# Performance work log

Measured on AMD Instinct MI355X. Metric: run time of the kernel, lower is better.

## Reference

```python
import jax, jax.numpy as jnp
import numpy as np

N_HEADS = 16
D_EMBED = 1024
HEAD_DIM = D_EMBED // N_HEADS


def setup_inputs() -> dict:
    key = jax.random.key(0)
    ks = jax.random.split(key, 9)
    s = 1.0 / np.sqrt(D_EMBED)
    def lin(kw, kb):
        W = jax.random.uniform(kw, (D_EMBED, D_EMBED), jnp.float32, -s, s)
        b = jax.random.uniform(kb, (D_EMBED,), jnp.float32, -s, s)
        return W, b
    q_w, q_b = lin(ks[0], ks[1])
    k_w, k_b = lin(ks[2], ks[3])
    v_w, v_b = lin(ks[4], ks[5])
    o_w, o_b = lin(ks[6], ks[7])
    x = jax.random.normal(ks[8], (4, 2048, D_EMBED), jnp.float32)
    return {"x": x, "q_w": q_w, "q_b": q_b, "k_w": k_w, "k_b": k_b,
            "v_w": v_w, "v_b": v_b, "o_w": o_w, "o_b": o_b}


def reference(x, q_w, q_b, k_w, k_b, v_w, v_b, o_w, o_b):
    B, S, _ = x.shape
    # projections; W stored as [in, out] so y = x @ W + b (matches nn.Linear math)
    def split_heads(y):
        return y.reshape(B, S, N_HEADS, HEAD_DIM).transpose(0, 2, 1, 3)  # [B,H,S,D]
    q = split_heads(x @ q_w + q_b)
    k = split_heads(x @ k_w + k_b)
    v = split_heads(x @ v_w + v_b)
    scale = 1.0 / np.sqrt(HEAD_DIM).astype(np.float32)
    scores = jnp.einsum('bhqd,bhkd->bhqk', q, k) * scale  # [B,H,S,S]
    weights = jax.nn.softmax(scores, axis=-1)
    attn = jnp.einsum('bhqk,bhkd->bhqd', weights, v)  # [B,H,S,D]
    attn = attn.transpose(0, 2, 1, 3).reshape(B, S, D_EMBED)
    return attn @ o_w + o_b
```

## Files before the change

kernel.cpp:

```cpp
#include <hip/hip_runtime.h>
#include <hip/hip_bf16.h>
#include <math.h>

typedef __attribute__((ext_vector_type(8))) short bf16x8;
typedef __attribute__((ext_vector_type(4))) float f32x4;

#define D_EMBED 1024
#define SEQ 2048
#define NH 16
#define HD 64
#define QSCALE 0.1803368801111204f

__device__ __forceinline__ short f2bf(float f) {
    union { float f; unsigned u; } v; v.f = f;
    return (short)((v.u + 0x7FFFu + ((v.u >> 16) & 1u)) >> 16);
}

__device__ __forceinline__ unsigned pk_bf16(float a, float b) {
#if __has_builtin(__builtin_amdgcn_cvt_pk_bf16_f32)
    typedef __attribute__((ext_vector_type(2))) __bf16 vbf2;
    union { vbf2 v; unsigned u; } c;
    c.v = __builtin_amdgcn_cvt_pk_bf16_f32(a, b);
    return c.u;
#else
    return (unsigned)(unsigned short)f2bf(a) | ((unsigned)(unsigned short)f2bf(b) << 16);
#endif
}

__device__ __forceinline__ float exp2f_(float x) {
#if __has_builtin(__builtin_amdgcn_exp2f)
    return __builtin_amdgcn_exp2f(x);
#else
    return __expf(x * 0.6931471805599453f);
#endif
}

typedef __attribute__((address_space(1))) const void gvoid_t;
typedef __attribute__((address_space(3))) void lvoid_t;
__device__ __forceinline__ void glds16(const void* g, void* l) {
    __builtin_amdgcn_global_load_lds((gvoid_t*)g, (lvoid_t*)l, 16, 0, 0);
}

__global__ __launch_bounds__(256) void xconv_kernel(const float* __restrict__ x,
                                                    short* __restrict__ xb)
{
    size_t i = ((size_t)blockIdx.x * 256 + threadIdx.x) * 8;
    float4 f0 = *(const float4*)(x + i);
    float4 f1 = *(const float4*)(x + i + 4);
    uint4 o;
    o.x = pk_bf16(f0.x, f0.y); o.y = pk_bf16(f0.z, f0.w);
    o.z = pk_bf16(f1.x, f1.y); o.w = pk_bf16(f1.z, f1.w);
    *(uint4*)(xb + i) = o;
}

__global__ __launch_bounds__(256) void wtrans_kernel(
    const float* __restrict__ w0, const float* __restrict__ w1,
    const float* __restrict__ w2, const float* __restrict__ w3,
    short* __restrict__ wt)
{
    __shared__ float tile[64][65];
    const float* W = (blockIdx.z == 0) ? w0 : (blockIdx.z == 1) ? w1
                   : (blockIdx.z == 2) ? w2 : w3;
    short* out = wt + (size_t)blockIdx.z * D_EMBED * D_EMBED;
    int k0 = blockIdx.x * 64, n0 = blockIdx.y * 64;
    #pragma unroll
    for (int i = 0; i < 16; i++) {
        int idx = threadIdx.x + i * 256; int r = idx >> 6, c = idx & 63;
        tile[r][c] = W[(size_t)(k0 + r) * D_EMBED + n0 + c];
    }
    __syncthreads();
    #pragma unroll
    for (int i = 0; i < 16; i++) {
        int idx = threadIdx.x + i * 256; int r = idx >> 6, c = idx & 63;
        out[(size_t)(n0 + r) * D_EMBED + k0 + c] = f2bf(tile[c][r]);
    }
}

__global__ __launch_bounds__(256) void gemm_qkv_kernel(
    const short* __restrict__ xb, const short* __restrict__ wt,
    const float* __restrict__ qb, const float* __restrict__ kb, const float* __restrict__ vb,
    short* __restrict__ qo, short* __restrict__ ko, short* __restrict__ vto)
{
    __shared__ __attribute__((aligned(16))) short As[128][32];
    __shared__ __attribute__((aligned(16))) short Bs[128][32];
    __shared__ __attribute__((aligned(16))) short Es[64][136];
    const int tid = threadIdx.x;
    const int lane = tid & 63, wv = tid >> 6;
    const int l16 = lane & 15, quad = lane >> 4;
    const int wm = (wv & 1) * 64, wn = (wv >> 1) * 64;
    const int m0 = blockIdx.y * 128, n0 = blockIdx.x * 128;

    const short* aptr0 = xb + (size_t)(m0 + (tid >> 2)) * D_EMBED + (tid & 3) * 8;
    const short* aptr1 = aptr0 + (size_t)64 * D_EMBED;
    const short* bptr0 = wt + (size_t)(n0 + (tid >> 2)) * D_EMBED + (tid & 3) * 8;
    const short* bptr1 = bptr0 + (size_t)64 * D_EMBED;
    char* aldsb = (char*)&As[0][0] + wv * 1024;
    char* bldsb = (char*)&Bs[0][0] + wv * 1024;

    f32x4 acc[4][4];
    #pragma unroll
    for (int a = 0; a < 4; a++)
        #pragma unroll
        for (int b = 0; b < 4; b++) acc[a][b] = (f32x4){0.f, 0.f, 0.f, 0.f};

    for (int k0 = 0; k0 < D_EMBED; k0 += 32) {
        __syncthreads();
        glds16(aptr0 + k0, aldsb);
        glds16(aptr1 + k0, aldsb + 4096);
        glds16(bptr0 + k0, bldsb);
        glds16(bptr1 + k0, bldsb + 4096);
        __syncthreads();
        bf16x8 af[4], bfr[4];
        #pragma unroll
        for (int mi = 0; mi < 4; mi++) af[mi]  = *(const bf16x8*)&As[wm + mi * 16 + l16][quad * 8];
        #pragma unroll
        for (int ni = 0; ni < 4; ni++) bfr[ni] = *(const bf16x8*)&Bs[wn + ni * 16 + l16][quad * 8];
        #pragma unroll
        for (int mi = 0; mi < 4; mi++)
            #pragma unroll
            for (int ni = 0; ni < 4; ni++)
                acc[mi][ni] = __builtin_amdgcn_mfma_f32_16x16x32_bf16(af[mi], bfr[ni], acc[mi][ni], 0, 0, 0);
    }

    const int zz = n0 >> 10;
    if (zz == 2) {
        const int b = m0 >> 11, st0 = m0 & 2047;
        const int hbase = (n0 & 1023) >> 6;
        #pragma unroll
        for (int h2 = 0; h2 < 2; h2++) {
            __syncthreads();
            if ((wv >> 1) == h2) {
                #pragma unroll
                for (int mi = 0; mi < 4; mi++) {
                    int sbase = (wv & 1) * 64 + mi * 16 + quad * 4;
                    #pragma unroll
                    for (int ni = 0; ni < 4; ni++) {
                        int d = ni * 16 + l16;
                        float bv = vb[(n0 & 1023) + h2 * 64 + d];
                        uint2 pw;
                        pw.x = pk_bf16(acc[mi][ni][0] + bv, acc[mi][ni][1] + bv);
                        pw.y = pk_bf16(acc[mi][ni][2] + bv, acc[mi][ni][3] + bv);
                        *(uint2*)&Es[d][sbase] = pw;
                    }
                }
            }
            __syncthreads();
            const int h = hbase + h2;
            #pragma unroll
            for (int j = 0; j < 4; j++) {
                int d = j * 16 + (tid >> 4);
                int sc = (tid & 15) * 8;
                bf16x8 vv = *(const bf16x8*)&Es[d][sc];
                *(bf16x8*)(vto + ((size_t)(b * NH + h) * HD + d) * SEQ + st0 + sc) = vv;
            }
        }
    } else {
        const int ncol0 = (n0 & 1023) + wn;
        const float* bias = (zz == 0) ? qb : kb;
        #pragma unroll
        for (int mi = 0; mi < 4; mi++)
            #pragma unroll
            for (int ni = 0; ni < 4; ni++)
                #pragma unroll
                for (int rg = 0; rg < 4; rg++) {
                    int row = m0 + wm + mi * 16 + quad * 4 + rg;
                    int col = ncol0 + ni * 16 + l16;
                    float v = acc[mi][ni][rg] + bias[col];
                    int b = row >> 11, s = row & 2047, h = col >> 6, d = col & 63;
                    if (zz == 0) qo[(((size_t)(b * NH + h)) * SEQ + s) * HD + d] = f2bf(v * QSCALE);
                    else         ko[(((size_t)(b * NH + h)) * SEQ + s) * HD + d] = f2bf(v);
                }
    }
}

__global__ __launch_bounds__(256) void flash_kernel(
    const short* __restrict__ Q, const short* __restrict__ K,
    const short* __restrict__ Vt, short* __restrict__ attn,
    short* __restrict__ Op0, short* __restrict__ Op1,
    float* __restrict__ lp0, float* __restrict__ lp1,
    int ktn, int mode)
{
    __shared__ __attribute__((aligned(16))) short Ks[64][64];
    __shared__ __attribute__((aligned(16))) short Vs[64][64];
    __shared__ __attribute__((aligned(16))) short Ps[4][64][72];
    const int bh = blockIdx.y, qt = blockIdx.x;
    const int kt0 = blockIdx.z * ktn;
    const int tid = threadIdx.x, lane = tid & 63, wv = tid >> 6;
    const int l16 = lane & 15, quad = lane >> 4;
    const int sw = l16 & 7;

    bf16x8 qf[4][2];
    #pragma unroll
    for (int g = 0; g < 4; g++) {
        const short* qp = Q + ((size_t)bh * SEQ + qt * 256 + wv * 64 + g * 16 + l16) * HD;
        qf[g][0] = *(const bf16x8*)(qp + quad * 8);
        qf[g][1] = *(const bf16x8*)(qp + 32 + quad * 8);
    }

    const int sr = tid >> 3;
    const int scg = (tid & 7) ^ (sr & 7);
    const short* kp0 = K  + ((size_t)bh * SEQ + sr) * HD + scg * 8;
    const short* vp0 = Vt + ((size_t)bh * HD + sr) * SEQ + scg * 8;
    char* kldsb = (char*)&Ks[0][0] + wv * 1024;
    char* vldsb = (char*)&Vs[0][0] + wv * 1024;

    float lsum[4] = {0.f, 0.f, 0.f, 0.f};
    f32x4 oacc[4][4];
    #pragma unroll
    for (int g = 0; g < 4; g++)
        #pragma unroll
        for (int di = 0; di < 4; di++) oacc[g][di] = (f32x4){0.f, 0.f, 0.f, 0.f};

    for (int kt = kt0; kt < kt0 + ktn; kt += 64) {
        __syncthreads();
        glds16(kp0 + (size_t)kt * HD, kldsb);
        glds16(kp0 + (size_t)(kt + 32) * HD, kldsb + 4096);
        glds16(vp0 + kt, vldsb);
        glds16(vp0 + (size_t)32 * SEQ + kt, vldsb + 4096);
        __syncthreads();

        bf16x8 kf[4][2];
        #pragma unroll
        for (int ni = 0; ni < 4; ni++) {
            kf[ni][0] = *(const bf16x8*)&Ks[ni * 16 + l16][((quad    ) ^ sw) * 8];
            kf[ni][1] = *(const bf16x8*)&Ks[ni * 16 + l16][((quad + 4) ^ sw) * 8];
        }

        #pragma unroll
        for (int g = 0; g < 4; g++) {
            f32x4 sacc[4];
            #pragma unroll
            for (int ni = 0; ni < 4; ni++) {
                sacc[ni] = (f32x4){0.f, 0.f, 0.f, 0.f};
                sacc[ni] = __builtin_amdgcn_mfma_f32_16x16x32_bf16(kf[ni][0], qf[g][0], sacc[ni], 0, 0, 0);
                sacc[ni] = __builtin_amdgcn_mfma_f32_16x16x32_bf16(kf[ni][1], qf[g][1], sacc[ni], 0, 0, 0);
            }
            short* prow = &Ps[wv][g * 16 + l16][0];
            float ps = 0.f;
            #pragma unroll
            for (int ni = 0; ni < 4; ni++) {
                float p0 = exp2f_(sacc[ni][0]);
                float p1 = exp2f_(sacc[ni][1]);
                float p2 = exp2f_(sacc[ni][2]);
                float p3 = exp2f_(sacc[ni][3]);
                ps += (p0 + p1) + (p2 + p3);
                uint2 pw; pw.x = pk_bf16(p0, p1); pw.y = pk_bf16(p2, p3);
                *(uint2*)(prow + ni * 16 + quad * 4) = pw;
            }
            lsum[g] += ps;
        }

        bf16x8 vf[4][2];
        #pragma unroll
        for (int di = 0; di < 4; di++) {
            vf[di][0] = *(const bf16x8*)&Vs[di * 16 + l16][((quad    ) ^ sw) * 8];
            vf[di][1] = *(const bf16x8*)&Vs[di * 16 + l16][((quad + 4) ^ sw) * 8];
        }
        #pragma unroll
        for (int g = 0; g < 4; g++) {
            const short* prow = &Ps[wv][g * 16 + l16][0];
            bf16x8 pf0 = *(const bf16x8*)(prow + quad * 8);
            bf16x8 pf1 = *(const bf16x8*)(prow + 32 + quad * 8);
            #pragma unroll
            for (int di = 0; di < 4; di++) {
                oacc[g][di] = __builtin_amdgcn_mfma_f32_16x16x32_bf16(pf0, vf[di][0], oacc[g][di], 0, 0, 0);
                oacc[g][di] = __builtin_amdgcn_mfma_f32_16x16x32_bf16(pf1, vf[di][1], oacc[g][di], 0, 0, 0);
            }
        }
    }

    const int b = bh >> 4, h = bh & 15;
    short* Oz = blockIdx.z ? Op1 : Op0;
    float* lz = blockIdx.z ? lp1 : lp0;
    #pragma unroll
    for (int g = 0; g < 4; g++) {
        float l = lsum[g];
        l += __shfl_xor(l, 16);
        l += __shfl_xor(l, 32);
        if (mode) {
            if (quad == 0) lz[(size_t)bh * SEQ + qt * 256 + wv * 64 + g * 16 + l16] = l;
            #pragma unroll
            for (int di = 0; di < 4; di++)
                #pragma unroll
                for (int rg = 0; rg < 4; rg++) {
                    int s = qt * 256 + wv * 64 + g * 16 + quad * 4 + rg;
                    int col = h * HD + di * 16 + l16;
                    Oz[((size_t)b * SEQ + s) * D_EMBED + col] = f2bf(oacc[g][di][rg]);
                }
        } else {
            float rl[4];
            #pragma unroll
            for (int rg = 0; rg < 4; rg++) rl[rg] = 1.0f / __shfl(l, quad * 4 + rg);
            #pragma unroll
            for (int di = 0; di < 4; di++)
                #pragma unroll
                for (int rg = 0; rg < 4; rg++) {
                    int s = qt * 256 + wv * 64 + g * 16 + quad * 4 + rg;
                    int col = h * HD + di * 16 + l16;
                    attn[((size_t)b * SEQ + s) * D_EMBED + col] = f2bf(oacc[g][di][rg] * rl[rg]);
                }
        }
    }
}

__global__ __launch_bounds__(256) void combine_kernel(
    const short* __restrict__ Op0, const short* __restrict__ Op1,
    const float* __restrict__ lp0, const float* __restrict__ lp1,
    short* __restrict__ attn)
{
    size_t i = (size_t)blockIdx.x * 256 + threadIdx.x;
    int r = (int)(i >> 7);
    int c8 = ((int)i & 127) * 8;
    int h = c8 >> 6, b = r >> 11, s = r & 2047;
    float l = lp0[(size_t)(b * NH + h) * SEQ + s] + lp1[(size_t)(b * NH + h) * SEQ + s];
    float rl = 1.0f / l;
    uint4 a0 = *(const uint4*)(Op0 + i * 8);
    uint4 a1 = *(const uint4*)(Op1 + i * 8);
    uint4 o;
    unsigned ua[4] = {a0.x, a0.y, a0.z, a0.w};
    unsigned ub[4] = {a1.x, a1.y, a1.z, a1.w};
    unsigned uo[4];
    #pragma unroll
    for (int j = 0; j < 4; j++) {
        union { unsigned u; float f; } f0l, f0h, f1l, f1h;
        f0l.u = (ua[j] & 0xffffu) << 16; f0h.u = ua[j] & 0xffff0000u;
        f1l.u = (ub[j] & 0xffffu) << 16; f1h.u = ub[j] & 0xffff0000u;
        uo[j] = pk_bf16((f0l.f + f1l.f) * rl, (f0h.f + f1h.f) * rl);
    }
    o.x = uo[0]; o.y = uo[1]; o.z = uo[2]; o.w = uo[3];
    *(uint4*)(attn + i * 8) = o;
}

__global__ __launch_bounds__(256) void gemm_out_kernel(
    const short* __restrict__ attn, const short* __restrict__ wt_o,
    const float* __restrict__ ob, float* __restrict__ out)
{
    __shared__ __attribute__((aligned(16))) short As[128][32];
    __shared__ __attribute__((aligned(16))) short Bs[128][32];
    const int tid = threadIdx.x;
    const int lane = tid & 63, wv = tid >> 6;
    const int l16 = lane & 15, quad = lane >> 4;
    const int wm = (wv & 1) * 64, wn = (wv >> 1) * 64;
    const int m0 = blockIdx.y * 128, n0 = blockIdx.x * 128;

    const short* aptr0 = attn + (size_t)(m0 + (tid >> 2)) * D_EMBED + (tid & 3) * 8;
    const short* aptr1 = aptr0 + (size_t)64 * D_EMBED;
    const short* bptr0 = wt_o + (size_t)(n0 + (tid >> 2)) * D_EMBED + (tid & 3) * 8;
    const short* bptr1 = bptr0 + (size_t)64 * D_EMBED;
    char* aldsb = (char*)&As[0][0] + wv * 1024;
    char* bldsb = (char*)&Bs[0][0] + wv * 1024;

    f32x4 acc[4][4];
    #pragma unroll
    for (int a = 0; a < 4; a++)
        #pragma unroll
        for (int b = 0; b < 4; b++) acc[a][b] = (f32x4){0.f, 0.f, 0.f, 0.f};

    for (int k0 = 0; k0 < D_EMBED; k0 += 32) {
        __syncthreads();
        glds16(aptr0 + k0, aldsb);
        glds16(aptr1 + k0, aldsb + 4096);
        glds16(bptr0 + k0, bldsb);
        glds16(bptr1 + k0, bldsb + 4096);
        __syncthreads();
        bf16x8 af[4], bfr[4];
        #pragma unroll
        for (int mi = 0; mi < 4; mi++) af[mi]  = *(const bf16x8*)&As[wm + mi * 16 + l16][quad * 8];
        #pragma unroll
        for (int ni = 0; ni < 4; ni++) bfr[ni] = *(const bf16x8*)&Bs[wn + ni * 16 + l16][quad * 8];
        #pragma unroll
        for (int mi = 0; mi < 4; mi++)
            #pragma unroll
            for (int ni = 0; ni < 4; ni++)
                acc[mi][ni] = __builtin_amdgcn_mfma_f32_16x16x32_bf16(af[mi], bfr[ni], acc[mi][ni], 0, 0, 0);
    }

    #pragma unroll
    for (int mi = 0; mi < 4; mi++)
        #pragma unroll
        for (int ni = 0; ni < 4; ni++)
            #pragma unroll
            for (int rg = 0; rg < 4; rg++) {
                int row = m0 + wm + mi * 16 + quad * 4 + rg;
                int col = n0 + wn + ni * 16 + l16;
                out[(size_t)row * D_EMBED + col] = acc[mi][ni][rg] + ob[col];
            }
}

extern "C" void kernel_launch(void* const* d_in, const int* in_sizes, int n_in,
                              void* d_out, int out_size, void* d_ws, size_t ws_size,
                              hipStream_t stream) {
    const float* x  = (const float*)d_in[0];
    const float* qw = (const float*)d_in[1];
    const float* qb = (const float*)d_in[2];
    const float* kw = (const float*)d_in[3];
    const float* kb = (const float*)d_in[4];
    const float* vw = (const float*)d_in[5];
    const float* vb = (const float*)d_in[6];
    const float* ow = (const float*)d_in[7];
    const float* ob = (const float*)d_in[8];

    char* ws = (char*)d_ws;
    short* xb  = (short*)(ws);
    short* wt  = (short*)(ws + (size_t)(16 << 20));
    short* q   = (short*)(ws + (size_t)(24 << 20));
    short* k   = (short*)(ws + (size_t)(40 << 20));
    short* vt  = (short*)(ws + (size_t)(56 << 20));
    short* at  = xb;

    const bool split = ws_size >= (size_t)105 * 1024 * 1024;
    short* Op0 = (short*)(ws + (size_t)(72 << 20));
    short* Op1 = (short*)(ws + (size_t)(88 << 20));
    float* lp0 = (float*)(ws + (size_t)(104 << 20));
    float* lp1 = (float*)(ws + (size_t)(104 << 20) + SEQ * 64 * sizeof(float));

    xconv_kernel<<<4096, 256, 0, stream>>>(x, xb);
    wtrans_kernel<<<dim3(16, 16, 4), 256, 0, stream>>>(qw, kw, vw, ow, wt);
    gemm_qkv_kernel<<<dim3(24, 64), 256, 0, stream>>>(xb, wt, qb, kb, vb, q, k, vt);
    if (split) {
        flash_kernel<<<dim3(8, 64, 2), 256, 0, stream>>>(q, k, vt, at, Op0, Op1, lp0, lp1,
                                                         SEQ / 2, 1);
        combine_kernel<<<(8192 * 1024 / 8) / 256, 256, 0, stream>>>(Op0, Op1, lp0, lp1, at);
    } else {
        flash_kernel<<<dim3(8, 64, 1), 256, 0, stream>>>(q, k, vt, at, at, at, lp0, lp0,
                                                         SEQ, 0);
    }
    gemm_out_kernel<<<dim3(8, 64), 256, 0, stream>>>(at, wt + (size_t)3 * D_EMBED * D_EMBED, ob, (float*)d_out);
}
```

Baseline: 317.6 us.

## Double-buffer K/V tiles in flash kernel and keep P in registers via permlane swaps

Adds a second LDS buffer for K and V so the next tile's async global-to-LDS loads are issued before the current tile's compute, which removes one barrier per iteration and overlaps loads with MFMA. The P tile no longer goes through an LDS round trip. Packed bf16 probabilities are rearranged into the PV MFMA operand layout with permlane32/permlane16 swaps (shuffle fallback if unavailable). The cost is more LDS for the two buffers and some extra register pressure from holding V fragments for the whole iteration.

```diff
diff --git a/kernel.cpp b/kernel.cpp
--- a/kernel.cpp
+++ b/kernel.cpp
@@ -32,6 +32,33 @@
     return __builtin_amdgcn_exp2f(x);
 #else
     return __expf(x * 0.6931471805599453f);
+#endif
+}
+
+__device__ __forceinline__ void pl32swap(unsigned &a, unsigned &b) {
+#if __has_builtin(__builtin_amdgcn_permlane32_swap)
+    auto r = __builtin_amdgcn_permlane32_swap(a, b, false, false);
+    a = r[0]; b = r[1];
+#else
+    unsigned ax = (unsigned)__shfl_xor((int)a, 32);
+    unsigned bx = (unsigned)__shfl_xor((int)b, 32);
+    bool hi = ((threadIdx.x & 63) >= 32);
+    unsigned na = hi ? bx : a;
+    unsigned nb = hi ? b : ax;
+    a = na; b = nb;
+#endif
+}
+__device__ __forceinline__ void pl16swap(unsigned &a, unsigned &b) {
+#if __has_builtin(__builtin_amdgcn_permlane16_swap)
+    auto r = __builtin_amdgcn_permlane16_swap(a, b, false, false);
+    a = r[0]; b = r[1];
+#else
+    unsigned ax = (unsigned)__shfl_xor((int)a, 16);
+    unsigned bx = (unsigned)__shfl_xor((int)b, 16);
+    bool odd = (((threadIdx.x >> 4) & 1) != 0);
+    unsigned na = odd ? bx : a;
+    unsigned nb = odd ? b : ax;
+    a = na; b = nb;
 #endif
 }
 
@@ -180,9 +207,8 @@
     float* __restrict__ lp0, float* __restrict__ lp1,
     int ktn, int mode)
 {
-    __shared__ __attribute__((aligned(16))) short Ks[64][64];
-    __shared__ __attribute__((aligned(16))) short Vs[64][64];
-    __shared__ __attribute__((aligned(16))) short Ps[4][64][72];
+    __shared__ __attribute__((aligned(16))) short Ks[2][64][64];
+    __shared__ __attribute__((aligned(16))) short Vs[2][64][64];
     const int bh = blockIdx.y, qt = blockIdx.x;
     const int kt0 = blockIdx.z * ktn;
     const int tid = threadIdx.x, lane = tid & 63, wv = tid >> 6;
@@ -201,8 +227,7 @@
     const int scg = (tid & 7) ^ (sr & 7);
     const short* kp0 = K  + ((size_t)bh * SEQ + sr) * HD + scg * 8;
     const short* vp0 = Vt + ((size_t)bh * HD + sr) * SEQ + scg * 8;
-    char* kldsb = (char*)&Ks[0][0] + wv * 1024;
-    char* vldsb = (char*)&Vs[0][0] + wv * 1024;
+    const int ldsoff = wv * 1024;
 
     float lsum[4] = {0.f, 0.f, 0.f, 0.f};
     f32x4 oacc[4][4];
@@ -211,19 +236,37 @@
         #pragma unroll
         for (int di = 0; di < 4; di++) oacc[g][di] = (f32x4){0.f, 0.f, 0.f, 0.f};
 
+    {
+        char* kb = (char*)&Ks[0][0][0] + ldsoff;
+        char* vbp = (char*)&Vs[0][0][0] + ldsoff;
+        glds16(kp0 + (size_t)kt0 * HD, kb);
+        glds16(kp0 + (size_t)(kt0 + 32) * HD, kb + 4096);
+        glds16(vp0 + kt0, vbp);
+        glds16(vp0 + (size_t)32 * SEQ + kt0, vbp + 4096);
+    }
+    __syncthreads();
+
+    int cur = 0;
     for (int kt = kt0; kt < kt0 + ktn; kt += 64) {
-        __syncthreads();
-        glds16(kp0 + (size_t)kt * HD, kldsb);
-        glds16(kp0 + (size_t)(kt + 32) * HD, kldsb + 4096);
-        glds16(vp0 + kt, vldsb);
-        glds16(vp0 + (size_t)32 * SEQ + kt, vldsb + 4096);
-        __syncthreads();
-
-        bf16x8 kf[4][2];
+        if (kt + 64 < kt0 + ktn) {
+            char* kb = (char*)&Ks[cur ^ 1][0][0] + ldsoff;
+            char* vbp = (char*)&Vs[cur ^ 1][0][0] + ldsoff;
+            glds16(kp0 + (size_t)(kt + 64) * HD, kb);
+            glds16(kp0 + (size_t)(kt + 96) * HD, kb + 4096);
+            glds16(vp0 + kt + 64, vbp);
+            glds16(vp0 + (size_t)32 * SEQ + kt + 64, vbp + 4096);
+        }
+
+        bf16x8 kf[4][2], vf[4][2];
         #pragma unroll
         for (int ni = 0; ni < 4; ni++) {
-            kf[ni][0] = *(const bf16x8*)&Ks[ni * 16 + l16][((quad    ) ^ sw) * 8];
-            kf[ni][1] = *(const bf16x8*)&Ks[ni * 16 + l16][((quad + 4) ^ sw) * 8];
+            kf[ni][0] = *(const bf16x8*)&Ks[cur][ni * 16 + l16][((quad    ) ^ sw) * 8];
+            kf[ni][1] = *(const bf16x8*)&Ks[cur][ni * 16 + l16][((quad + 4) ^ sw) * 8];
+        }
+        #pragma unroll
+        for (int di = 0; di < 4; di++) {
+            vf[di][0] = *(const bf16x8*)&Vs[cur][di * 16 + l16][((quad    ) ^ sw) * 8];
+            vf[di][1] = *(const bf16x8*)&Vs[cur][di * 16 + l16][((quad + 4) ^ sw) * 8];
         }
 
         #pragma unroll
@@ -235,7 +278,7 @@
                 sacc[ni] = __builtin_amdgcn_mfma_f32_16x16x32_bf16(kf[ni][0], qf[g][0], sacc[ni], 0, 0, 0);
                 sacc[ni] = __builtin_amdgcn_mfma_f32_16x16x32_bf16(kf[ni][1], qf[g][1], sacc[ni], 0, 0, 0);
             }
-            short* prow = &Ps[wv][g * 16 + l16][0];
+            unsigned w[4][2];
             float ps = 0.f;
             #pragma unroll
             for (int ni = 0; ni < 4; ni++) {
@@ -244,29 +287,25 @@
                 float p2 = exp2f_(sacc[ni][2]);
                 float p3 = exp2f_(sacc[ni][3]);
                 ps += (p0 + p1) + (p2 + p3);
-                uint2 pw; pw.x = pk_bf16(p0, p1); pw.y = pk_bf16(p2, p3);
-                *(uint2*)(prow + ni * 16 + quad * 4) = pw;
+                w[ni][0] = pk_bf16(p0, p1);
+                w[ni][1] = pk_bf16(p2, p3);
             }
             lsum[g] += ps;
-        }
-
-        bf16x8 vf[4][2];
-        #pragma unroll
-        for (int di = 0; di < 4; di++) {
-            vf[di][0] = *(const bf16x8*)&Vs[di * 16 + l16][((quad    ) ^ sw) * 8];
-            vf[di][1] = *(const bf16x8*)&Vs[di * 16 + l16][((quad + 4) ^ sw) * 8];
-        }
-        #pragma unroll
-        for (int g = 0; g < 4; g++) {
-            const short* prow = &Ps[wv][g * 16 + l16][0];
-            bf16x8 pf0 = *(const bf16x8*)(prow + quad * 8);
-            bf16x8 pf1 = *(const bf16x8*)(prow + 32 + quad * 8);
-            #pragma unroll
-            for (int di = 0; di < 4; di++) {
-                oacc[g][di] = __builtin_amdgcn_mfma_f32_16x16x32_bf16(pf0, vf[di][0], oacc[g][di], 0, 0, 0);
-                oacc[g][di] = __builtin_amdgcn_mfma_f32_16x16x32_bf16(pf1, vf[di][1], oacc[g][di], 0, 0, 0);
-            }
-        }
+            #pragma unroll
+            for (int h = 0; h < 2; h++) {
+                unsigned a0 = w[2 * h][0], b0 = w[2 * h + 1][0];
+                unsigned a1 = w[2 * h][1], b1 = w[2 * h + 1][1];
+                pl32swap(a0, b0); pl32swap(a1, b1);
+                pl16swap(a0, b0); pl16swap(a1, b1);
+                union { unsigned u[4]; bf16x8 v; } pu;
+                pu.u[0] = a0; pu.u[1] = a1; pu.u[2] = b0; pu.u[3] = b1;
+                #pragma unroll
+                for (int di = 0; di < 4; di++)
+                    oacc[g][di] = __builtin_amdgcn_mfma_f32_16x16x32_bf16(pu.v, vf[di][h], oacc[g][di], 0, 0, 0);
+            }
+        }
+        __syncthreads();
+        cur ^= 1;
     }
 
     const int b = bh >> 4, h = bh & 15;
```

After: 341.7 us. 7.6% more time.
